# Kernel tuning notes

Hardware: AMD Instinct MI355X
Metric: run time of the kernel (lower is better)

The kernel has to match this reference:

```python
import jax, jax.numpy as jnp
import numpy as np

B, C, N, K, COUT = 2, 192, 16384, 16, 192
EPS = 1e-5


def setup_inputs() -> dict:
    key = jax.random.key(0)
    k1, k2, k3 = jax.random.split(key, 3)
    x = jax.random.normal(k1, (B, C, N, 1), dtype=jnp.float32)
    edge_index = jax.random.randint(k2, (2, B, N, K), 0, N, dtype=jnp.int32)
    # kaiming-normal-ish 1x1 conv weight, flattened to [C_out, 2C]
    W = jax.random.normal(k3, (COUT, 2 * C), dtype=jnp.float32) * np.float32(np.sqrt(2.0 / (2 * C)))
    b_conv = jnp.zeros((COUT,), jnp.float32)
    gamma = jnp.ones((COUT,), jnp.float32)
    beta = jnp.zeros((COUT,), jnp.float32)
    return {"x": x, "W": W, "b_conv": b_conv, "gamma": gamma, "beta": beta, "edge_index": edge_index}


def reference(x, W, b_conv, gamma, beta, edge_index):
    b, c, n, _ = x.shape
    k = edge_index.shape[-1]
    xs = x[..., 0]  # [B,C,N]

    def gather(idx):  # idx: [B,N,K] -> [B,C,N,K]
        return jnp.take_along_axis(xs, idx.reshape(b, 1, n * k), axis=2).reshape(b, c, n, k)

    x_i = gather(edge_index[1])
    x_j = gather(edge_index[0])
    mr = jnp.max(x_j - x_i, axis=-1)  # max-relative feature [B,C,N]

    # torch.cat([x.unsqueeze(2), x_j.unsqueeze(2)], 2).reshape(b, 2c, n, 1) interleaves channels
    cat = jnp.stack([xs, mr], axis=2).reshape(b, 2 * c, n)  # [B,2C,N]

    # 1x1 conv == channel matmul
    h = jnp.einsum('oc,bcn->bon', W, cat) + b_conv[None, :, None]  # [B,COUT,N]

    # BatchNorm2d (training-mode batch statistics over batch+spatial dims)
    mean = h.mean(axis=(0, 2), keepdims=True)
    var = h.var(axis=(0, 2), keepdims=True)
    h = (h - mean) / jnp.sqrt(var + EPS) * gamma[None, :, None] + beta[None, :, None]

    out = jax.nn.gelu(h, approximate=False)
    return out[..., None]  # [B,COUT,N,1]
```

## Files before the change

### kernel.cpp

```cpp
#include <hip/hip_runtime.h>
#include <math.h>

#define BB 2
#define CC 192
#define NN 16384
#define KK 16
#define COUT 192
#define MM (BB * NN)
#define KDIM (2 * CC)
#define EPSF 1e-5f
#define NGB 256

typedef __attribute__((ext_vector_type(8))) short short8;
typedef __attribute__((ext_vector_type(4))) float f32x4;

#define AS1P const __attribute__((address_space(1))) void*
#define AS3P __attribute__((address_space(3))) void*

static __device__ __forceinline__ float bf16_to_f32(unsigned int u16) {
    return __uint_as_float(u16 << 16);
}
static __device__ __forceinline__ float bf16hi_to_f32(unsigned int u) {
    return __uint_as_float(u & 0xffff0000u);
}
static __device__ __forceinline__ unsigned short f32_to_bf16(float f) {
    unsigned int u = __float_as_uint(f);
    unsigned int r = (u + 0x7fffu + ((u >> 16) & 1u)) >> 16;
    return (unsigned short)r;
}
static __device__ __forceinline__ float gelu_exact(float v) {
    return 0.5f * v * (1.0f + erff(v * 0.70710678118654752440f));
}

#define TRB (512 * 3 * BB)
__global__ __launch_bounds__(256) void k_prep(const float* __restrict__ x,
                                              unsigned int* __restrict__ xt32,
                                              const float* __restrict__ W,
                                              unsigned short* __restrict__ Wb) {
    int bid = blockIdx.x;
    int t = threadIdx.x;
    if (bid >= TRB) {
        int wb = bid - TRB;
        int base = wb * 1024 + t * 4;
        float4 v = *(const float4*)(W + base);
        uint2 o;
        o.x = (unsigned int)f32_to_bf16(v.x) | ((unsigned int)f32_to_bf16(v.y) << 16);
        o.y = (unsigned int)f32_to_bf16(v.z) | ((unsigned int)f32_to_bf16(v.w) << 16);
        *(uint2*)(Wb + base) = o;
        return;
    }
    __shared__ float tile[64][33];
    int nb = bid & 511;
    int rest = bid >> 9;
    int cb = rest % 3;
    int b = rest / 3;
    int n0 = nb * 32, c0 = cb * 64;
    int tx = t & 31, ty = t >> 5;
    #pragma unroll
    for (int j = 0; j < 64; j += 8)
        tile[ty + j][tx] = x[((size_t)b * CC + (c0 + ty + j)) * NN + n0 + tx];
    __syncthreads();
    int c = c0 + 2 * tx;
    int chunk = c / 48, wi = c % 48;
    #pragma unroll
    for (int j = 0; j < 32; j += 8) {
        int n = n0 + ty + j;
        unsigned int w = (unsigned int)f32_to_bf16(tile[2 * tx][ty + j]) |
                         ((unsigned int)f32_to_bf16(tile[2 * tx + 1][ty + j]) << 16);
        xt32[((size_t)(b * 4 + chunk) * NN + n) * 24 + wi / 2] = w;
    }
}

__global__ __launch_bounds__(384) void k_gather(const unsigned short* __restrict__ xt4,
                                                const int* __restrict__ edge,
                                                uint4* __restrict__ xcat4) {
    __shared__ int sj[64 * KK], si[64 * KK];
    int bid = blockIdx.x;
    int combo = bid & 7;
    int g = bid >> 3;
    int b = combo >> 2, ch = combo & 3;
    int n0 = g * 64;
    int t = threadIdx.x;
    const int* ej = edge + ((size_t)b * NN + n0) * KK;
    const int* ei = edge + ((size_t)(BB + b) * NN + n0) * KK;
    for (int u = t; u < 64 * KK; u += 384) { sj[u] = ej[u]; si[u] = ei[u]; }
    __syncthreads();

    int p = t / 6, c4 = t % 6;
    const uint4* base = (const uint4*)(xt4 + (size_t)(b * 4 + ch) * NN * 48) + c4;
    float mx[8];
    #pragma unroll
    for (int c = 0; c < 8; ++c) mx[c] = -INFINITY;
    #pragma unroll
    for (int k = 0; k < KK; ++k) {
        uint4 vj = base[(size_t)sj[p * KK + k] * 6];
        uint4 vi = base[(size_t)si[p * KK + k] * 6];
        const unsigned int dj[4] = {vj.x, vj.y, vj.z, vj.w};
        const unsigned int di[4] = {vi.x, vi.y, vi.z, vi.w};
        #pragma unroll
        for (int d = 0; d < 4; ++d) {
            mx[2 * d]     = fmaxf(mx[2 * d],     bf16_to_f32(dj[d] & 0xffffu) - bf16_to_f32(di[d] & 0xffffu));
            mx[2 * d + 1] = fmaxf(mx[2 * d + 1], bf16hi_to_f32(dj[d]) - bf16hi_to_f32(di[d]));
        }
    }
    uint4 xs = base[(size_t)(n0 + p) * 6];
    uint4 o0, o1;
    o0.x = (xs.x & 0xffffu) | ((unsigned int)f32_to_bf16(mx[0]) << 16);
    o0.y = (xs.x >> 16)     | ((unsigned int)f32_to_bf16(mx[1]) << 16);
    o0.z = (xs.y & 0xffffu) | ((unsigned int)f32_to_bf16(mx[2]) << 16);
    o0.w = (xs.y >> 16)     | ((unsigned int)f32_to_bf16(mx[3]) << 16);
    o1.x = (xs.z & 0xffffu) | ((unsigned int)f32_to_bf16(mx[4]) << 16);
    o1.y = (xs.z >> 16)     | ((unsigned int)f32_to_bf16(mx[5]) << 16);
    o1.z = (xs.w & 0xffffu) | ((unsigned int)f32_to_bf16(mx[6]) << 16);
    o1.w = (xs.w >> 16)     | ((unsigned int)f32_to_bf16(mx[7]) << 16);
    size_t orow = (size_t)(b * NN + n0 + p) * 48;
    xcat4[orow + ch * 12 + 2 * c4]     = o0;
    xcat4[orow + ch * 12 + 2 * c4 + 1] = o1;
}

#define BMT 128
__global__ __launch_bounds__(512) void k_gemm(const unsigned short* __restrict__ xcat,
                                              const unsigned short* __restrict__ Wb,
                                              unsigned short* __restrict__ h,
                                              float* __restrict__ psum,
                                              float* __restrict__ psum2) {
    __shared__ __align__(16) char ldsA[BMT * 128];
    __shared__ __align__(16) char ldsB[COUT * 128];
    int t = threadIdx.x;
    int m0 = blockIdx.x * BMT;
    int w = t >> 6, l = t & 63, lo = l & 15, q4 = l >> 4;
    int lr = l >> 3, lc = l & 7;
    f32x4 acc[12];
    #pragma unroll
    for (int i = 0; i < 12; ++i) acc[i] = (f32x4){0.f, 0.f, 0.f, 0.f};
    int rA = w * 16 + lo;

    for (int ks = 0; ks < KDIM / 64; ++ks) {
        int k0 = ks * 64;
        if (ks) __syncthreads();
        #pragma unroll
        for (int e = 0; e < 2; ++e) {
            int r = w * 16 + e * 8 + lr;
            int cg = lc ^ (r & 7);
            const unsigned short* gp = xcat + (size_t)(m0 + r) * KDIM + k0 + cg * 8;
            __builtin_amdgcn_global_load_lds((AS1P)gp, (AS3P)(ldsA + w * 2048 + e * 1024), 16, 0, 0);
        }
        #pragma unroll
        for (int e = 0; e < 3; ++e) {
            int r = w * 24 + e * 8 + lr;
            int cg = lc ^ (r & 7);
            const unsigned short* gp = Wb + (size_t)r * KDIM + k0 + cg * 8;
            __builtin_amdgcn_global_load_lds((AS1P)gp, (AS3P)(ldsB + w * 3072 + e * 1024), 16, 0, 0);
        }
        __syncthreads();
        #pragma unroll
        for (int kh = 0; kh < 2; ++kh) {
            int cb = kh * 64 + q4 * 16;
            short8 a = *(const short8*)(ldsA + rA * 128 + (cb ^ ((rA & 7) << 4)));
            #pragma unroll
            for (int ot = 0; ot < 12; ++ot) {
                int rB = ot * 16 + lo;
                short8 bf = *(const short8*)(ldsB + rB * 128 + (cb ^ ((rB & 7) << 4)));
                acc[ot] = __builtin_amdgcn_mfma_f32_16x16x32_bf16(a, bf, acc[ot], 0, 0, 0);
            }
        }
    }
    __syncthreads();

    float* reds = (float*)ldsA;
    float* reds2 = reds + 8 * COUT;
    int mrow = m0 + w * 16 + q4 * 4;
    #pragma unroll
    for (int ot = 0; ot < 12; ++ot) {
        int o = ot * 16 + lo;
        float s = 0.f, s2 = 0.f;
        #pragma unroll
        for (int r = 0; r < 4; ++r) {
            float v = acc[ot][r];
            h[(size_t)(mrow + r) * COUT + o] = f32_to_bf16(v);
            s += v;
            s2 += v * v;
        }
        s += __shfl_xor(s, 16);  s2 += __shfl_xor(s2, 16);
        s += __shfl_xor(s, 32);  s2 += __shfl_xor(s2, 32);
        if (q4 == 0) {
            reds[w * COUT + o] = s;
            reds2[w * COUT + o] = s2;
        }
    }
    __syncthreads();
    if (t < COUT) {
        float a = 0.f, a2 = 0.f;
        #pragma unroll
        for (int w8 = 0; w8 < 8; ++w8) {
            a += reds[w8 * COUT + t];
            a2 += reds2[w8 * COUT + t];
        }
        psum[blockIdx.x * COUT + t] = a;
        psum2[blockIdx.x * COUT + t] = a2;
    }
}

__global__ __launch_bounds__(256) void k_bn(const float* __restrict__ psum,
                                            const float* __restrict__ psum2,
                                            const float* __restrict__ gamma,
                                            const float* __restrict__ beta,
                                            float* __restrict__ sc_sh) {
    __shared__ float red[2][32][8];
    int t = threadIdx.x;
    int ch = t & 7, rr = t >> 3;
    int o = blockIdx.x * 8 + ch;
    float a = 0.f, a2 = 0.f;
    for (int r = rr; r < NGB; r += 32) {
        a += psum[r * COUT + o];
        a2 += psum2[r * COUT + o];
    }
    red[0][rr][ch] = a;
    red[1][rr][ch] = a2;
    __syncthreads();
    if (t < 8) {
        float s = 0.f, s2 = 0.f;
        #pragma unroll
        for (int i = 0; i < 32; ++i) { s += red[0][i][t]; s2 += red[1][i][t]; }
        int oo = blockIdx.x * 8 + t;
        float inv_m = 1.0f / (float)MM;
        float mean = s * inv_m;
        float var = s2 * inv_m - mean * mean;
        float sc = gamma[oo] * rsqrtf(var + EPSF);
        sc_sh[oo] = sc;
        sc_sh[COUT + oo] = beta[oo] - mean * sc;
    }
}

__global__ __launch_bounds__(256) void k_out(const unsigned short* __restrict__ h,
                                             const float* __restrict__ sc_sh,
                                             float* __restrict__ out) {
    __shared__ float tile[64][36];
    int b = blockIdx.z;
    int n0 = blockIdx.x * 64;
    int o0 = blockIdx.y * 32;
    int t = threadIdx.x;
    {
        int r = t >> 2, c4 = t & 3;
        uint4 hv = *(const uint4*)(h + ((size_t)b * NN + n0 + r) * COUT + o0 + c4 * 8);
        const unsigned int d[4] = {hv.x, hv.y, hv.z, hv.w};
        #pragma unroll
        for (int e = 0; e < 4; ++e) {
            int oc = c4 * 8 + 2 * e;
            float v0 = bf16_to_f32(d[e] & 0xffffu) * sc_sh[o0 + oc] + sc_sh[COUT + o0 + oc];
            float v1 = bf16hi_to_f32(d[e]) * sc_sh[o0 + oc + 1] + sc_sh[COUT + o0 + oc + 1];
            tile[r][oc] = gelu_exact(v0);
            tile[r][oc + 1] = gelu_exact(v1);
        }
    }
    __syncthreads();
    int o = t >> 3, q = t & 7;
    #pragma unroll
    for (int it = 0; it < 2; ++it) {
        int nn = q * 4 + it * 32;
        float4 v = {tile[nn][o], tile[nn + 1][o], tile[nn + 2][o], tile[nn + 3][o]};
        *(float4*)(out + ((size_t)b * COUT + o0 + o) * NN + n0 + nn) = v;
    }
}

extern "C" void kernel_launch(void* const* d_in, const int* in_sizes, int n_in,
                              void* d_out, int out_size, void* d_ws, size_t ws_size,
                              hipStream_t stream) {
    const float* x = (const float*)d_in[0];
    const float* W = (const float*)d_in[1];
    const float* gamma = (const float*)d_in[3];
    const float* beta = (const float*)d_in[4];
    const int* edge = (const int*)d_in[5];
    float* out = (float*)d_out;

    char* ws = (char*)d_ws;
    unsigned short* xt4 = (unsigned short*)ws;
    ws += (size_t)MM * CC * 2;
    unsigned short* xcat = (unsigned short*)ws;
    ws += (size_t)MM * KDIM * 2;
    unsigned short* Wb = (unsigned short*)ws;
    ws += (size_t)COUT * KDIM * 2;
    unsigned short* h = (unsigned short*)ws;
    ws += (size_t)MM * COUT * 2;
    float* psum = (float*)ws;
    ws += (size_t)NGB * COUT * sizeof(float);
    float* psum2 = (float*)ws;
    ws += (size_t)NGB * COUT * sizeof(float);
    float* sc_sh = (float*)ws;

    k_prep<<<TRB + 72, 256, 0, stream>>>(x, (unsigned int*)xt4, W, Wb);

    k_gather<<<8 * (NN / 64), 384, 0, stream>>>(xt4, edge, (uint4*)xcat);

    k_gemm<<<MM / BMT, 512, 0, stream>>>(xcat, Wb, h, psum, psum2);

    k_bn<<<24, 256, 0, stream>>>(psum, psum2, gamma, beta, sc_sh);

    dim3 ogrid(NN / 64, COUT / 32, BB);
    k_out<<<ogrid, dim3(256), 0, stream>>>(h, sc_sh, out);
}
```

Before: 73.81 us.

## Fuse gather max-relative into GEMM kernel with row-major bf16 x layout

```diff
diff --git a/kernel.cpp b/kernel.cpp
--- a/kernel.cpp
+++ b/kernel.cpp
@@ -60,74 +60,92 @@
     for (int j = 0; j < 64; j += 8)
         tile[ty + j][tx] = x[((size_t)b * CC + (c0 + ty + j)) * NN + n0 + tx];
     __syncthreads();
-    int c = c0 + 2 * tx;
-    int chunk = c / 48, wi = c % 48;
     #pragma unroll
     for (int j = 0; j < 32; j += 8) {
         int n = n0 + ty + j;
         unsigned int w = (unsigned int)f32_to_bf16(tile[2 * tx][ty + j]) |
                          ((unsigned int)f32_to_bf16(tile[2 * tx + 1][ty + j]) << 16);
-        xt32[((size_t)(b * 4 + chunk) * NN + n) * 24 + wi / 2] = w;
-    }
-}
-
-__global__ __launch_bounds__(384) void k_gather(const unsigned short* __restrict__ xt4,
-                                                const int* __restrict__ edge,
-                                                uint4* __restrict__ xcat4) {
-    __shared__ int sj[64 * KK], si[64 * KK];
-    int bid = blockIdx.x;
-    int combo = bid & 7;
-    int g = bid >> 3;
-    int b = combo >> 2, ch = combo & 3;
-    int n0 = g * 64;
-    int t = threadIdx.x;
-    const int* ej = edge + ((size_t)b * NN + n0) * KK;
-    const int* ei = edge + ((size_t)(BB + b) * NN + n0) * KK;
-    for (int u = t; u < 64 * KK; u += 384) { sj[u] = ej[u]; si[u] = ei[u]; }
-    __syncthreads();
-
-    int p = t / 6, c4 = t % 6;
-    const uint4* base = (const uint4*)(xt4 + (size_t)(b * 4 + ch) * NN * 48) + c4;
-    float mx[8];
-    #pragma unroll
-    for (int c = 0; c < 8; ++c) mx[c] = -INFINITY;
-    #pragma unroll
-    for (int k = 0; k < KK; ++k) {
-        uint4 vj = base[(size_t)sj[p * KK + k] * 6];
-        uint4 vi = base[(size_t)si[p * KK + k] * 6];
-        const unsigned int dj[4] = {vj.x, vj.y, vj.z, vj.w};
-        const unsigned int di[4] = {vi.x, vi.y, vi.z, vi.w};
-        #pragma unroll
-        for (int d = 0; d < 4; ++d) {
-            mx[2 * d]     = fmaxf(mx[2 * d],     bf16_to_f32(dj[d] & 0xffffu) - bf16_to_f32(di[d] & 0xffffu));
-            mx[2 * d + 1] = fmaxf(mx[2 * d + 1], bf16hi_to_f32(dj[d]) - bf16hi_to_f32(di[d]));
-        }
-    }
-    uint4 xs = base[(size_t)(n0 + p) * 6];
-    uint4 o0, o1;
-    o0.x = (xs.x & 0xffffu) | ((unsigned int)f32_to_bf16(mx[0]) << 16);
-    o0.y = (xs.x >> 16)     | ((unsigned int)f32_to_bf16(mx[1]) << 16);
-    o0.z = (xs.y & 0xffffu) | ((unsigned int)f32_to_bf16(mx[2]) << 16);
-    o0.w = (xs.y >> 16)     | ((unsigned int)f32_to_bf16(mx[3]) << 16);
-    o1.x = (xs.z & 0xffffu) | ((unsigned int)f32_to_bf16(mx[4]) << 16);
-    o1.y = (xs.z >> 16)     | ((unsigned int)f32_to_bf16(mx[5]) << 16);
-    o1.z = (xs.w & 0xffffu) | ((unsigned int)f32_to_bf16(mx[6]) << 16);
-    o1.w = (xs.w >> 16)     | ((unsigned int)f32_to_bf16(mx[7]) << 16);
-    size_t orow = (size_t)(b * NN + n0 + p) * 48;
-    xcat4[orow + ch * 12 + 2 * c4]     = o0;
-    xcat4[orow + ch * 12 + 2 * c4 + 1] = o1;
+        xt32[(((size_t)b * NN + n) * CC + c0) / 2 + tx] = w;
+    }
 }
 
 #define BMT 128
-__global__ __launch_bounds__(512) void k_gemm(const unsigned short* __restrict__ xcat,
-                                              const unsigned short* __restrict__ Wb,
-                                              unsigned short* __restrict__ h,
-                                              float* __restrict__ psum,
-                                              float* __restrict__ psum2) {
+__global__ __launch_bounds__(512) void k_fused(const unsigned short* __restrict__ xt,
+                                               const int* __restrict__ edge,
+                                               const unsigned short* __restrict__ Wb,
+                                               unsigned short* __restrict__ xcat,
+                                               unsigned short* __restrict__ h,
+                                               float* __restrict__ psum,
+                                               float* __restrict__ psum2) {
     __shared__ __align__(16) char ldsA[BMT * 128];
     __shared__ __align__(16) char ldsB[COUT * 128];
+    __shared__ unsigned short sjw[BMT * KK], siw[BMT * KK];
     int t = threadIdx.x;
     int m0 = blockIdx.x * BMT;
+    int b = m0 >> 14, n0 = m0 & (NN - 1);
+
+    {
+        const int* ej = edge + ((size_t)b * NN + n0) * KK;
+        const int* ei = edge + ((size_t)(BB + b) * NN + n0) * KK;
+        for (int u = t; u < BMT * KK; u += 512) {
+            sjw[u] = (unsigned short)ej[u];
+            siw[u] = (unsigned short)ei[u];
+        }
+    }
+    __syncthreads();
+
+    {
+        int q = t & 7;
+        const uint4* rowb = (const uint4*)(xt + (size_t)b * NN * CC);
+        uint4* xc4 = (uint4*)xcat;
+        #pragma unroll
+        for (int g2 = 0; g2 < 2; ++g2) {
+            int p = g2 * 64 + (t >> 3);
+            float mx[24];
+            #pragma unroll
+            for (int c = 0; c < 24; ++c) mx[c] = -INFINITY;
+            #pragma unroll
+            for (int k = 0; k < KK; ++k) {
+                int rj = sjw[p * KK + k];
+                int ri = siw[p * KK + k];
+                const uint4* pj = rowb + (size_t)rj * 24 + q * 3;
+                const uint4* pi = rowb + (size_t)ri * 24 + q * 3;
+                #pragma unroll
+                for (int s = 0; s < 3; ++s) {
+                    uint4 vj = pj[s], vi = pi[s];
+                    const unsigned int dj[4] = {vj.x, vj.y, vj.z, vj.w};
+                    const unsigned int di[4] = {vi.x, vi.y, vi.z, vi.w};
+                    #pragma unroll
+                    for (int d = 0; d < 4; ++d) {
+                        mx[s * 8 + 2 * d]     = fmaxf(mx[s * 8 + 2 * d],
+                            bf16_to_f32(dj[d] & 0xffffu) - bf16_to_f32(di[d] & 0xffffu));
+                        mx[s * 8 + 2 * d + 1] = fmaxf(mx[s * 8 + 2 * d + 1],
+                            bf16hi_to_f32(dj[d]) - bf16hi_to_f32(di[d]));
+                    }
+                }
+            }
+            const uint4* px = rowb + (size_t)(n0 + p) * 24 + q * 3;
+            size_t orow = (size_t)(m0 + p) * 48 + q * 6;
+            #pragma unroll
+            for (int s = 0; s < 3; ++s) {
+                uint4 xsv = px[s];
+                const unsigned int dx[4] = {xsv.x, xsv.y, xsv.z, xsv.w};
+                uint4 o0, o1;
+                o0.x = (dx[0] & 0xffffu) | ((unsigned int)f32_to_bf16(mx[s * 8 + 0]) << 16);
+                o0.y = (dx[0] >> 16)     | ((unsigned int)f32_to_bf16(mx[s * 8 + 1]) << 16);
+                o0.z = (dx[1] & 0xffffu) | ((unsigned int)f32_to_bf16(mx[s * 8 + 2]) << 16);
+                o0.w = (dx[1] >> 16)     | ((unsigned int)f32_to_bf16(mx[s * 8 + 3]) << 16);
+                o1.x = (dx[2] & 0xffffu) | ((unsigned int)f32_to_bf16(mx[s * 8 + 4]) << 16);
+                o1.y = (dx[2] >> 16)     | ((unsigned int)f32_to_bf16(mx[s * 8 + 5]) << 16);
+                o1.z = (dx[3] & 0xffffu) | ((unsigned int)f32_to_bf16(mx[s * 8 + 6]) << 16);
+                o1.w = (dx[3] >> 16)     | ((unsigned int)f32_to_bf16(mx[s * 8 + 7]) << 16);
+                xc4[orow + 2 * s]     = o0;
+                xc4[orow + 2 * s + 1] = o1;
+            }
+        }
+    }
+    __syncthreads();
+
     int w = t >> 6, l = t & 63, lo = l & 15, q4 = l >> 4;
     int lr = l >> 3, lc = l & 7;
     f32x4 acc[12];
@@ -274,7 +292,7 @@
     float* out = (float*)d_out;
 
     char* ws = (char*)d_ws;
-    unsigned short* xt4 = (unsigned short*)ws;
+    unsigned short* xt = (unsigned short*)ws;
     ws += (size_t)MM * CC * 2;
     unsigned short* xcat = (unsigned short*)ws;
     ws += (size_t)MM * KDIM * 2;
@@ -288,11 +306,9 @@
     ws += (size_t)NGB * COUT * sizeof(float);
     float* sc_sh = (float*)ws;
 
-    k_prep<<<TRB + 72, 256, 0, stream>>>(x, (unsigned int*)xt4, W, Wb);
-
-    k_gather<<<8 * (NN / 64), 384, 0, stream>>>(xt4, edge, (uint4*)xcat);
-
-    k_gemm<<<MM / BMT, 512, 0, stream>>>(xcat, Wb, h, psum, psum2);
+    k_prep<<<TRB + 72, 256, 0, stream>>>(x, (unsigned int*)xt, W, Wb);
+
+    k_fused<<<MM / BMT, 512, 0, stream>>>(xt, edge, Wb, xcat, h, psum, psum2);
 
     k_bn<<<24, 256, 0, stream>>>(psum, psum2, gamma, beta, sc_sh);
 
```

New measurement: 84.37 us. 14.3% more time.

## Make gather persistent with XCC-affine work stealing per batch-channel combo

Applied to the files above, without the earlier changes.

```diff
diff --git a/kernel.cpp b/kernel.cpp
--- a/kernel.cpp
+++ b/kernel.cpp
@@ -10,6 +10,7 @@
 #define KDIM (2 * CC)
 #define EPSF 1e-5f
 #define NGB 256
+#define NGRP (NN / 64)
 
 typedef __attribute__((ext_vector_type(8))) short short8;
 typedef __attribute__((ext_vector_type(4))) float f32x4;
@@ -36,11 +37,13 @@
 __global__ __launch_bounds__(256) void k_prep(const float* __restrict__ x,
                                               unsigned int* __restrict__ xt32,
                                               const float* __restrict__ W,
-                                              unsigned short* __restrict__ Wb) {
+                                              unsigned short* __restrict__ Wb,
+                                              int* __restrict__ ctr) {
     int bid = blockIdx.x;
     int t = threadIdx.x;
     if (bid >= TRB) {
         int wb = bid - TRB;
+        if (wb == 0 && t < 16) ctr[t] = 0;
         int base = wb * 1024 + t * 4;
         float4 v = *(const float4*)(W + base);
         uint2 o;
@@ -73,49 +76,72 @@
 
 __global__ __launch_bounds__(384) void k_gather(const unsigned short* __restrict__ xt4,
                                                 const int* __restrict__ edge,
-                                                uint4* __restrict__ xcat4) {
-    __shared__ int sj[64 * KK], si[64 * KK];
-    int bid = blockIdx.x;
-    int combo = bid & 7;
-    int g = bid >> 3;
-    int b = combo >> 2, ch = combo & 3;
-    int n0 = g * 64;
-    int t = threadIdx.x;
-    const int* ej = edge + ((size_t)b * NN + n0) * KK;
-    const int* ei = edge + ((size_t)(BB + b) * NN + n0) * KK;
-    for (int u = t; u < 64 * KK; u += 384) { sj[u] = ej[u]; si[u] = ei[u]; }
-    __syncthreads();
-
-    int p = t / 6, c4 = t % 6;
-    const uint4* base = (const uint4*)(xt4 + (size_t)(b * 4 + ch) * NN * 48) + c4;
-    float mx[8];
-    #pragma unroll
-    for (int c = 0; c < 8; ++c) mx[c] = -INFINITY;
-    #pragma unroll
-    for (int k = 0; k < KK; ++k) {
-        uint4 vj = base[(size_t)sj[p * KK + k] * 6];
-        uint4 vi = base[(size_t)si[p * KK + k] * 6];
-        const unsigned int dj[4] = {vj.x, vj.y, vj.z, vj.w};
-        const unsigned int di[4] = {vi.x, vi.y, vi.z, vi.w};
-        #pragma unroll
-        for (int d = 0; d < 4; ++d) {
-            mx[2 * d]     = fmaxf(mx[2 * d],     bf16_to_f32(dj[d] & 0xffffu) - bf16_to_f32(di[d] & 0xffffu));
-            mx[2 * d + 1] = fmaxf(mx[2 * d + 1], bf16hi_to_f32(dj[d]) - bf16hi_to_f32(di[d]));
-        }
-    }
-    uint4 xs = base[(size_t)(n0 + p) * 6];
-    uint4 o0, o1;
-    o0.x = (xs.x & 0xffffu) | ((unsigned int)f32_to_bf16(mx[0]) << 16);
-    o0.y = (xs.x >> 16)     | ((unsigned int)f32_to_bf16(mx[1]) << 16);
-    o0.z = (xs.y & 0xffffu) | ((unsigned int)f32_to_bf16(mx[2]) << 16);
-    o0.w = (xs.y >> 16)     | ((unsigned int)f32_to_bf16(mx[3]) << 16);
-    o1.x = (xs.z & 0xffffu) | ((unsigned int)f32_to_bf16(mx[4]) << 16);
-    o1.y = (xs.z >> 16)     | ((unsigned int)f32_to_bf16(mx[5]) << 16);
-    o1.z = (xs.w & 0xffffu) | ((unsigned int)f32_to_bf16(mx[6]) << 16);
-    o1.w = (xs.w >> 16)     | ((unsigned int)f32_to_bf16(mx[7]) << 16);
-    size_t orow = (size_t)(b * NN + n0 + p) * 48;
-    xcat4[orow + ch * 12 + 2 * c4]     = o0;
-    xcat4[orow + ch * 12 + 2 * c4 + 1] = o1;
+                                                uint4* __restrict__ xcat4,
+                                                int* __restrict__ ctr) {
+    __shared__ unsigned short sj[64 * KK], si[64 * KK];
+    __shared__ int s_g;
+    int t = threadIdx.x;
+    unsigned xcc = __builtin_amdgcn_s_getreg((3 << 11) | 20) & 7;
+
+    for (int a = 0; a < 8; ++a) {
+        int combo = (int)((xcc + a) & 7);
+        if (a > 0) {
+            if (blockIdx.x >= 256) break;
+            __syncthreads();
+            if (t == 0) s_g = *(volatile const int*)(ctr + combo);
+            __syncthreads();
+            if (s_g >= NGRP) continue;
+        }
+        while (true) {
+            __syncthreads();
+            if (t == 0) s_g = atomicAdd(ctr + combo, 1);
+            __syncthreads();
+            int g = s_g;
+            if (g >= NGRP) break;
+
+            int b = combo >> 2, ch = combo & 3;
+            int n0 = g * 64;
+            const int* ej = edge + ((size_t)b * NN + n0) * KK;
+            const int* ei = edge + ((size_t)(BB + b) * NN + n0) * KK;
+            for (int u = t; u < 64 * KK; u += 384) {
+                sj[u] = (unsigned short)ej[u];
+                si[u] = (unsigned short)ei[u];
+            }
+            __syncthreads();
+
+            int p = t / 6, c4 = t % 6;
+            const uint4* base = (const uint4*)(xt4 + (size_t)(b * 4 + ch) * NN * 48) + c4;
+            float mx[8];
+            #pragma unroll
+            for (int c = 0; c < 8; ++c) mx[c] = -INFINITY;
+            #pragma unroll
+            for (int k = 0; k < KK; ++k) {
+                uint4 vj = base[(size_t)sj[p * KK + k] * 6];
+                uint4 vi = base[(size_t)si[p * KK + k] * 6];
+                const unsigned int dj[4] = {vj.x, vj.y, vj.z, vj.w};
+                const unsigned int di[4] = {vi.x, vi.y, vi.z, vi.w};
+                #pragma unroll
+                for (int d = 0; d < 4; ++d) {
+                    mx[2 * d]     = fmaxf(mx[2 * d],     bf16_to_f32(dj[d] & 0xffffu) - bf16_to_f32(di[d] & 0xffffu));
+                    mx[2 * d + 1] = fmaxf(mx[2 * d + 1], bf16hi_to_f32(dj[d]) - bf16hi_to_f32(di[d]));
+                }
+            }
+            uint4 xs = base[(size_t)(n0 + p) * 6];
+            uint4 o0, o1;
+            o0.x = (xs.x & 0xffffu) | ((unsigned int)f32_to_bf16(mx[0]) << 16);
+            o0.y = (xs.x >> 16)     | ((unsigned int)f32_to_bf16(mx[1]) << 16);
+            o0.z = (xs.y & 0xffffu) | ((unsigned int)f32_to_bf16(mx[2]) << 16);
+            o0.w = (xs.y >> 16)     | ((unsigned int)f32_to_bf16(mx[3]) << 16);
+            o1.x = (xs.z & 0xffffu) | ((unsigned int)f32_to_bf16(mx[4]) << 16);
+            o1.y = (xs.z >> 16)     | ((unsigned int)f32_to_bf16(mx[5]) << 16);
+            o1.z = (xs.w & 0xffffu) | ((unsigned int)f32_to_bf16(mx[6]) << 16);
+            o1.w = (xs.w >> 16)     | ((unsigned int)f32_to_bf16(mx[7]) << 16);
+            size_t orow = (size_t)(b * NN + n0 + p) * 48;
+            xcat4[orow + ch * 12 + 2 * c4]     = o0;
+            xcat4[orow + ch * 12 + 2 * c4 + 1] = o1;
+            __syncthreads();
+        }
+    }
 }
 
 #define BMT 128
@@ -287,10 +313,12 @@
     float* psum2 = (float*)ws;
     ws += (size_t)NGB * COUT * sizeof(float);
     float* sc_sh = (float*)ws;
-
-    k_prep<<<TRB + 72, 256, 0, stream>>>(x, (unsigned int*)xt4, W, Wb);
-
-    k_gather<<<8 * (NN / 64), 384, 0, stream>>>(xt4, edge, (uint4*)xcat);
+    ws += 2 * COUT * sizeof(float);
+    int* ctr = (int*)ws;
+
+    k_prep<<<TRB + 72, 256, 0, stream>>>(x, (unsigned int*)xt4, W, Wb, ctr);
+
+    k_gather<<<2048, 384, 0, stream>>>(xt4, edge, (uint4*)xcat, ctr);
 
     k_gemm<<<MM / BMT, 512, 0, stream>>>(xcat, Wb, h, psum, psum2);
 
```

Result: slower. 189.4 us (+156.6%).

## Store transposed x as full node rows and gather whole rows per node

Applied to the files above, without the earlier changes.

```diff
diff --git a/kernel.cpp b/kernel.cpp
--- a/kernel.cpp
+++ b/kernel.cpp
@@ -13,6 +13,7 @@
 
 typedef __attribute__((ext_vector_type(8))) short short8;
 typedef __attribute__((ext_vector_type(4))) float f32x4;
+typedef __attribute__((ext_vector_type(4))) unsigned int u32x4;
 
 #define AS1P const __attribute__((address_space(1))) void*
 #define AS3P __attribute__((address_space(3))) void*
@@ -58,43 +59,41 @@
     int tx = t & 31, ty = t >> 5;
     #pragma unroll
     for (int j = 0; j < 64; j += 8)
-        tile[ty + j][tx] = x[((size_t)b * CC + (c0 + ty + j)) * NN + n0 + tx];
-    __syncthreads();
-    int c = c0 + 2 * tx;
-    int chunk = c / 48, wi = c % 48;
+        tile[ty + j][tx] = __builtin_nontemporal_load(
+            &x[((size_t)b * CC + (c0 + ty + j)) * NN + n0 + tx]);
+    __syncthreads();
     #pragma unroll
     for (int j = 0; j < 32; j += 8) {
         int n = n0 + ty + j;
         unsigned int w = (unsigned int)f32_to_bf16(tile[2 * tx][ty + j]) |
                          ((unsigned int)f32_to_bf16(tile[2 * tx + 1][ty + j]) << 16);
-        xt32[((size_t)(b * 4 + chunk) * NN + n) * 24 + wi / 2] = w;
-    }
-}
-
-__global__ __launch_bounds__(384) void k_gather(const unsigned short* __restrict__ xt4,
+        xt32[(((size_t)b * NN + n) * CC + c0) / 2 + tx] = w;
+    }
+}
+
+__global__ __launch_bounds__(384) void k_gather(const unsigned short* __restrict__ xt,
                                                 const int* __restrict__ edge,
-                                                uint4* __restrict__ xcat4) {
-    __shared__ int sj[64 * KK], si[64 * KK];
-    int bid = blockIdx.x;
-    int combo = bid & 7;
-    int g = bid >> 3;
-    int b = combo >> 2, ch = combo & 3;
-    int n0 = g * 64;
-    int t = threadIdx.x;
-    const int* ej = edge + ((size_t)b * NN + n0) * KK;
-    const int* ei = edge + ((size_t)(BB + b) * NN + n0) * KK;
-    for (int u = t; u < 64 * KK; u += 384) { sj[u] = ej[u]; si[u] = ei[u]; }
-    __syncthreads();
-
-    int p = t / 6, c4 = t % 6;
-    const uint4* base = (const uint4*)(xt4 + (size_t)(b * 4 + ch) * NN * 48) + c4;
+                                                unsigned int* __restrict__ xcat32) {
+    __shared__ int sj[16][KK], si[16][KK];
+    int t = threadIdx.x;
+    int m0 = blockIdx.x * 16;
+    int b = m0 >> 14, n0 = m0 & (NN - 1);
+    if (t < 256)
+        ((int*)sj)[t] = __builtin_nontemporal_load(&edge[((size_t)b * NN + n0) * KK + t]);
+    if (t >= 128)
+        ((int*)si)[t - 128] = __builtin_nontemporal_load(
+            &edge[((size_t)(BB + b) * NN + n0) * KK + (t - 128)]);
+    __syncthreads();
+
+    int p = t / 24, c4 = t % 24;
+    const uint4* base = (const uint4*)(xt + (size_t)b * NN * CC) + c4;
     float mx[8];
     #pragma unroll
     for (int c = 0; c < 8; ++c) mx[c] = -INFINITY;
     #pragma unroll
     for (int k = 0; k < KK; ++k) {
-        uint4 vj = base[(size_t)sj[p * KK + k] * 6];
-        uint4 vi = base[(size_t)si[p * KK + k] * 6];
+        uint4 vj = base[(size_t)sj[p][k] * 24];
+        uint4 vi = base[(size_t)si[p][k] * 24];
         const unsigned int dj[4] = {vj.x, vj.y, vj.z, vj.w};
         const unsigned int di[4] = {vi.x, vi.y, vi.z, vi.w};
         #pragma unroll
@@ -103,8 +102,8 @@
             mx[2 * d + 1] = fmaxf(mx[2 * d + 1], bf16hi_to_f32(dj[d]) - bf16hi_to_f32(di[d]));
         }
     }
-    uint4 xs = base[(size_t)(n0 + p) * 6];
-    uint4 o0, o1;
+    uint4 xs = base[(size_t)(n0 + p) * 6 * 4];
+    u32x4 o0, o1;
     o0.x = (xs.x & 0xffffu) | ((unsigned int)f32_to_bf16(mx[0]) << 16);
     o0.y = (xs.x >> 16)     | ((unsigned int)f32_to_bf16(mx[1]) << 16);
     o0.z = (xs.y & 0xffffu) | ((unsigned int)f32_to_bf16(mx[2]) << 16);
@@ -113,9 +112,9 @@
     o1.y = (xs.z >> 16)     | ((unsigned int)f32_to_bf16(mx[5]) << 16);
     o1.z = (xs.w & 0xffffu) | ((unsigned int)f32_to_bf16(mx[6]) << 16);
     o1.w = (xs.w >> 16)     | ((unsigned int)f32_to_bf16(mx[7]) << 16);
-    size_t orow = (size_t)(b * NN + n0 + p) * 48;
-    xcat4[orow + ch * 12 + 2 * c4]     = o0;
-    xcat4[orow + ch * 12 + 2 * c4 + 1] = o1;
+    size_t obase = ((size_t)(m0 + p) * 48 + 2 * c4) * 4;
+    __builtin_nontemporal_store(o0, (u32x4*)(xcat32 + obase));
+    __builtin_nontemporal_store(o1, (u32x4*)(xcat32 + obase + 4));
 }
 
 #define BMT 128
@@ -258,8 +257,9 @@
     #pragma unroll
     for (int it = 0; it < 2; ++it) {
         int nn = q * 4 + it * 32;
-        float4 v = {tile[nn][o], tile[nn + 1][o], tile[nn + 2][o], tile[nn + 3][o]};
-        *(float4*)(out + ((size_t)b * COUT + o0 + o) * NN + n0 + nn) = v;
+        f32x4 v = {tile[nn][o], tile[nn + 1][o], tile[nn + 2][o], tile[nn + 3][o]};
+        __builtin_nontemporal_store(v,
+            (f32x4*)(out + ((size_t)b * COUT + o0 + o) * NN + n0 + nn));
     }
 }
 
@@ -274,7 +274,7 @@
     float* out = (float*)d_out;
 
     char* ws = (char*)d_ws;
-    unsigned short* xt4 = (unsigned short*)ws;
+    unsigned short* xt = (unsigned short*)ws;
     ws += (size_t)MM * CC * 2;
     unsigned short* xcat = (unsigned short*)ws;
     ws += (size_t)MM * KDIM * 2;
@@ -288,9 +288,9 @@
     ws += (size_t)NGB * COUT * sizeof(float);
     float* sc_sh = (float*)ws;
 
-    k_prep<<<TRB + 72, 256, 0, stream>>>(x, (unsigned int*)xt4, W, Wb);
-
-    k_gather<<<8 * (NN / 64), 384, 0, stream>>>(xt4, edge, (uint4*)xcat);
+    k_prep<<<TRB + 72, 256, 0, stream>>>(x, (unsigned int*)xt, W, Wb);
+
+    k_gather<<<MM / 16, 384, 0, stream>>>(xt, edge, (unsigned int*)xcat);
 
     k_gemm<<<MM / BMT, 512, 0, stream>>>(xcat, Wb, h, psum, psum2);
 
```

Result: no change. 75.18 us (+1.9%).
